# Kernel tuning notes

Hardware: AMD Instinct MI355X
Metric: run time of the kernel (lower is better)

## Reference

```python
import jax, jax.numpy as jnp
import numpy as np

N_NODES = 100000
N_EDGES = 50000
NNZ = 1600000
C_IN = 128
C_OUT = 128
BN_EPS = 1e-5


def setup_inputs() -> dict:
    key = jax.random.key(0)
    k_x, k_ni, k_ei, k_w, k_W, k_b = jax.random.split(key, 6)
    x = jax.random.normal(k_x, (N_NODES, C_IN), dtype=jnp.float32)
    node_idx = jax.random.randint(k_ni, (NNZ,), 0, N_NODES, dtype=jnp.int64)
    edge_idx = jax.random.randint(k_ei, (NNZ,), 0, N_EDGES, dtype=jnp.int64)
    hyperedge_index = jnp.stack([node_idx, edge_idx], axis=0)  # [2, nnz]
    hyperedge_weight = jax.random.uniform(k_w, (N_EDGES,), dtype=jnp.float32)
    W = jax.random.normal(k_W, (C_IN, C_OUT), dtype=jnp.float32) * (1.0 / np.sqrt(C_IN))
    b = jax.random.normal(k_b, (C_OUT,), dtype=jnp.float32) * 0.02
    gamma = jnp.ones((C_OUT,), dtype=jnp.float32)
    beta = jnp.zeros((C_OUT,), dtype=jnp.float32)
    return {"x": x, "hyperedge_index": hyperedge_index,
            "hyperedge_weight": hyperedge_weight, "W": W, "b": b,
            "gamma": gamma, "beta": beta}


def reference(x, hyperedge_index, hyperedge_weight, W, b, gamma, beta):
    # HypergraphConv (PyG semantics): out = D^{-1} H B^{-1} H^T (X W) + b
    # D_v = sum_{e: v in e} w_e  (hyperedge weights enter via node degree),
    # B_e = |e| (number of incident nodes).
    N = x.shape[0]
    E = hyperedge_weight.shape[0]
    node_idx = hyperedge_index[0]
    edge_idx = hyperedge_index[1]

    xt = x @ W  # [N, C_out]

    # Node degree D (weighted) and hyperedge degree B.
    D = jax.ops.segment_sum(hyperedge_weight[edge_idx], node_idx, num_segments=N)
    D_inv = jnp.where(D > 0, 1.0 / D, 0.0)  # inf -> 0
    Bdeg = jax.ops.segment_sum(jnp.ones(edge_idx.shape, dtype=xt.dtype),
                               edge_idx, num_segments=E)
    B_inv = jnp.where(Bdeg > 0, 1.0 / Bdeg, 0.0)

    # node -> hyperedge aggregation: e = B^{-1} sum_{v in e} xt_v
    e_feat = jax.ops.segment_sum(xt[node_idx], edge_idx, num_segments=E)
    e_feat = e_feat * B_inv[:, None]  # [E, C_out]

    # hyperedge -> node aggregation: out_v = D^{-1} sum_{e ni v} e_feat_e
    out = jax.ops.segment_sum(e_feat[edge_idx], node_idx, num_segments=N)
    out = out * D_inv[:, None] + b  # [N, C_out]

    # BatchNorm (training-mode batch statistics over nodes)
    mean = jnp.mean(out, axis=0)
    var = jnp.mean(jnp.square(out - mean), axis=0)  # biased, as BatchNorm1d
    out = (out - mean) * jax.lax.rsqrt(var + BN_EPS) * gamma + beta

    # SiLU activation
    out = out * jax.nn.sigmoid(out)
    # NOTE: original code computes `x = out + x` for the skip but returns `out`,
    # so the skip is a no-op; we faithfully return `out` (use_skip=False here).
    return out
```

## Files before the change

### kernel.cpp

```cpp
#include <hip/hip_runtime.h>
#include <cstdint>
#include <cstddef>

#define CC 128
#define LOG_FINE 7
#define FINE 128
#define CAPE 6144
#define CAPV 3072
#define BIN_TILE 8192

__device__ __forceinline__ unsigned f2b(float f) {
    const unsigned u = __float_as_uint(f);
    return (u + 0x7fffu + ((u >> 16) & 1u)) >> 16;
}
__device__ __forceinline__ float b2f_lo(unsigned u) { return __uint_as_float(u << 16); }
__device__ __forceinline__ float b2f_hi(unsigned u) { return __uint_as_float(u & 0xffff0000u); }

__global__ __launch_bounds__(512) void prep(const int* __restrict__ nidx,
                                            const int* __restrict__ eidx,
                                            int* __restrict__ curE,
                                            int* __restrict__ curV,
                                            unsigned* __restrict__ binnedE,
                                            unsigned* __restrict__ binnedV,
                                            int nnz, int nbE, int nbV, int nbin,
                                            const float4* __restrict__ xin,
                                            uint2* __restrict__ xh, int n4) {
    __shared__ int cntE[512], gposE[512];
    __shared__ int cntV[1024], gposV[1024];
    const int tid = threadIdx.x;
    if (blockIdx.x >= (unsigned)nbin) {
        const int bid = blockIdx.x - nbin;
        const int nblk = gridDim.x - nbin;
        for (int i = bid * 512 + tid; i < n4; i += nblk * 512) {
            const float4 v = xin[i];
            xh[i] = make_uint2(f2b(v.x) | (f2b(v.y) << 16), f2b(v.z) | (f2b(v.w) << 16));
        }
        return;
    }
    for (int i = tid; i < nbE; i += 512) cntE[i] = 0;
    for (int i = tid; i < nbV; i += 512) cntV[i] = 0;
    __syncthreads();
    const int base = blockIdx.x * BIN_TILE;
    int pE[16], rE[16], pV[16], rV[16];
#pragma unroll
    for (int j = 0; j < 16; ++j) {
        const int i = base + tid + j * 512;
        if (i < nnz) {
            const int e = eidx[i], v = nidx[i];
            const int bE = e >> LOG_FINE, bV = v >> LOG_FINE;
            rE[j] = (bE << 16) | atomicAdd(&cntE[bE], 1);
            pE[j] = (v << LOG_FINE) | (e & (FINE - 1));
            rV[j] = (bV << 16) | atomicAdd(&cntV[bV], 1);
            pV[j] = (e << LOG_FINE) | (v & (FINE - 1));
        } else { rE[j] = -1; rV[j] = -1; }
    }
    __syncthreads();
    for (int i = tid; i < nbE; i += 512) {
        const int c = cntE[i];
        gposE[i] = (c > 0) ? atomicAdd(&curE[i], c) : 0;
    }
    for (int i = tid; i < nbV; i += 512) {
        const int c = cntV[i];
        gposV[i] = (c > 0) ? atomicAdd(&curV[i], c) : 0;
    }
    __syncthreads();
#pragma unroll
    for (int j = 0; j < 16; ++j) {
        if (rE[j] >= 0) {
            const int b = rE[j] >> 16;
            binnedE[(size_t)b * CAPE + gposE[b] + (rE[j] & 0xffff)] = (unsigned)pE[j];
        }
        if (rV[j] >= 0) {
            const int b = rV[j] >> 16;
            binnedV[(size_t)b * CAPV + gposV[b] + (rV[j] & 0xffff)] = (unsigned)pV[j];
        }
    }
}

__global__ __launch_bounds__(512) void fill_fineE(const int* __restrict__ cur,
                                                  unsigned* __restrict__ binned,
                                                  int2* __restrict__ rows, int nrows) {
    __shared__ unsigned vals[CAPE];
    __shared__ int scnt[FINE], soff[FINE], sscan[FINE];
    const int tid = threadIdx.x;
    const int b = blockIdx.x;
    const int base = b * CAPE;
    const int cnt = cur[b];
    for (int i = tid; i < cnt; i += 512) vals[i] = binned[base + i];
    if (tid < FINE) scnt[tid] = 0;
    __syncthreads();
    for (int i = tid; i < cnt; i += 512) atomicAdd(&scnt[vals[i] & (FINE - 1)], 1);
    __syncthreads();
    if (tid < FINE) sscan[tid] = scnt[tid];
    __syncthreads();
#pragma unroll
    for (int d = 1; d < FINE; d <<= 1) {
        int t = 0;
        if (tid >= d && tid < FINE) t = sscan[tid - d];
        __syncthreads();
        if (tid < FINE) sscan[tid] += t;
        __syncthreads();
    }
    if (tid < FINE) {
        const int excl = sscan[tid] - scnt[tid];
        soff[tid] = excl;
        const int row = (b << LOG_FINE) + tid;
        if (row < nrows) rows[row] = make_int2(base + excl, base + excl + scnt[tid]);
    }
    __syncthreads();
    for (int i = tid; i < cnt; i += 512) {
        const unsigned p = vals[i];
        const int slot = (int)(p & (FINE - 1));
        const int pos = base + atomicAdd(&soff[slot], 1);
        binned[pos] = p >> LOG_FINE;
    }
}

__global__ __launch_bounds__(512) void fillV_gather(const int* __restrict__ curV,
                                                    unsigned* __restrict__ binnedV,
                                                    const float* __restrict__ hw,
                                                    int2* __restrict__ rowsV,
                                                    float* __restrict__ Dinv,
                                                    int N, int nbV,
                                                    const int2* __restrict__ rowsE,
                                                    const unsigned* __restrict__ binnedE,
                                                    const uint4* __restrict__ xh4,
                                                    uint4* __restrict__ eraw4, int E) {
    __shared__ unsigned vals[CAPV];
    __shared__ int scnt[FINE], soff[FINE], sscan[FINE];
    __shared__ float sd[FINE];
    const int tid = threadIdx.x;
    if (blockIdx.x < (unsigned)nbV) {
        const int b = blockIdx.x;
        const int base = b * CAPV;
        const int cnt = curV[b];
        for (int i = tid; i < cnt; i += 512) vals[i] = binnedV[base + i];
        if (tid < FINE) { scnt[tid] = 0; sd[tid] = 0.f; }
        __syncthreads();
        for (int i = tid; i < cnt; i += 512) atomicAdd(&scnt[vals[i] & (FINE - 1)], 1);
        __syncthreads();
        if (tid < FINE) sscan[tid] = scnt[tid];
        __syncthreads();
#pragma unroll
        for (int d = 1; d < FINE; d <<= 1) {
            int t = 0;
            if (tid >= d && tid < FINE) t = sscan[tid - d];
            __syncthreads();
            if (tid < FINE) sscan[tid] += t;
            __syncthreads();
        }
        if (tid < FINE) {
            const int excl = sscan[tid] - scnt[tid];
            soff[tid] = excl;
            const int row = (b << LOG_FINE) + tid;
            if (row < N) rowsV[row] = make_int2(base + excl, base + excl + scnt[tid]);
        }
        __syncthreads();
        for (int i = tid; i < cnt; i += 512) {
            const unsigned p = vals[i];
            const int slot = (int)(p & (FINE - 1));
            const int e = (int)(p >> LOG_FINE);
            const int pos = base + atomicAdd(&soff[slot], 1);
            binnedV[pos] = (unsigned)e;
            atomicAdd(&sd[slot], hw[e]);
        }
        __syncthreads();
        if (tid < FINE) {
            const int row = (b << LOG_FINE) + tid;
            if (row < N) {
                const float d = sd[tid];
                Dinv[row] = (d > 0.f) ? 1.f / d : 0.f;
            }
        }
        return;
    }
    const int sub = tid >> 5;
    const int half = (tid >> 4) & 1;
    const int q = tid & 15;
    const int e = (blockIdx.x - nbV) * 16 + sub;
    if (e >= E) return;
    const int2 st = rowsE[e];
    const int s = st.x, t = st.y;
    float a[8];
#pragma unroll
    for (int k = 0; k < 8; ++k) a[k] = 0.f;
    int j = s;
    for (; j + 7 < t; j += 8) {
        const int v0 = (int)binnedE[j + 0 + half];
        const int v1 = (int)binnedE[j + 2 + half];
        const int v2 = (int)binnedE[j + 4 + half];
        const int v3 = (int)binnedE[j + 6 + half];
        const uint4 u0 = xh4[(size_t)v0 * 16 + q];
        const uint4 u1 = xh4[(size_t)v1 * 16 + q];
        const uint4 u2 = xh4[(size_t)v2 * 16 + q];
        const uint4 u3 = xh4[(size_t)v3 * 16 + q];
        a[0] += b2f_lo(u0.x) + b2f_lo(u1.x) + b2f_lo(u2.x) + b2f_lo(u3.x);
        a[1] += b2f_hi(u0.x) + b2f_hi(u1.x) + b2f_hi(u2.x) + b2f_hi(u3.x);
        a[2] += b2f_lo(u0.y) + b2f_lo(u1.y) + b2f_lo(u2.y) + b2f_lo(u3.y);
        a[3] += b2f_hi(u0.y) + b2f_hi(u1.y) + b2f_hi(u2.y) + b2f_hi(u3.y);
        a[4] += b2f_lo(u0.z) + b2f_lo(u1.z) + b2f_lo(u2.z) + b2f_lo(u3.z);
        a[5] += b2f_hi(u0.z) + b2f_hi(u1.z) + b2f_hi(u2.z) + b2f_hi(u3.z);
        a[6] += b2f_lo(u0.w) + b2f_lo(u1.w) + b2f_lo(u2.w) + b2f_lo(u3.w);
        a[7] += b2f_hi(u0.w) + b2f_hi(u1.w) + b2f_hi(u2.w) + b2f_hi(u3.w);
    }
    for (; j + 1 < t; j += 2) {
        const int v0 = (int)binnedE[j + half];
        const uint4 u = xh4[(size_t)v0 * 16 + q];
        a[0] += b2f_lo(u.x); a[1] += b2f_hi(u.x);
        a[2] += b2f_lo(u.y); a[3] += b2f_hi(u.y);
        a[4] += b2f_lo(u.z); a[5] += b2f_hi(u.z);
        a[6] += b2f_lo(u.w); a[7] += b2f_hi(u.w);
    }
    if (j < t && half == 0) {
        const uint4 u = xh4[(size_t)binnedE[j] * 16 + q];
        a[0] += b2f_lo(u.x); a[1] += b2f_hi(u.x);
        a[2] += b2f_lo(u.y); a[3] += b2f_hi(u.y);
        a[4] += b2f_lo(u.z); a[5] += b2f_hi(u.z);
        a[6] += b2f_lo(u.w); a[7] += b2f_hi(u.w);
    }
#pragma unroll
    for (int k = 0; k < 8; ++k) a[k] += __shfl_xor(a[k], 16);
    if (half == 0) {
        const float binv = (t > s) ? 1.f / (float)(t - s) : 0.f;
#pragma unroll
        for (int k = 0; k < 8; ++k) a[k] *= binv;
        uint4 o;
        o.x = f2b(a[0]) | (f2b(a[1]) << 16);
        o.y = f2b(a[2]) | (f2b(a[3]) << 16);
        o.z = f2b(a[4]) | (f2b(a[5]) << 16);
        o.w = f2b(a[6]) | (f2b(a[7]) << 16);
        eraw4[(size_t)e * 16 + q] = o;
    }
}

__global__ __launch_bounds__(256) void mm_kernel(const unsigned* __restrict__ A,
                                                 const float* __restrict__ W,
                                                 unsigned* __restrict__ Out, int M) {
    __shared__ float Wl[CC * CC];
    __shared__ float Xl[32 * CC];
    const int tid = threadIdx.x;
    for (int i = tid * 4; i < CC * CC; i += 1024) {
        *(float4*)&Wl[i] = *(const float4*)&W[i];
    }
    const int row0 = blockIdx.x * 32;
    for (int i = tid; i < 2048; i += 256) {
        const int r = i >> 6;
        const int u = i & 63;
        const int row = row0 + r;
        const unsigned val = (row < M) ? A[(size_t)row * 64 + u] : 0u;
        Xl[r * CC + 2 * u]     = b2f_lo(val);
        Xl[r * CC + 2 * u + 1] = b2f_hi(val);
    }
    __syncthreads();
    const int c4 = (tid & 31) * 4;
    const int rg = tid >> 5;
    float4 acc[4];
#pragma unroll
    for (int r = 0; r < 4; ++r) acc[r] = make_float4(0.f, 0.f, 0.f, 0.f);
    for (int k4 = 0; k4 < 32; ++k4) {
        float4 xv[4];
#pragma unroll
        for (int r = 0; r < 4; ++r) xv[r] = *(const float4*)&Xl[(rg + r * 8) * CC + k4 * 4];
#pragma unroll
        for (int kk = 0; kk < 4; ++kk) {
            const float4 w = *(const float4*)&Wl[(k4 * 4 + kk) * CC + c4];
#pragma unroll
            for (int r = 0; r < 4; ++r) {
                const float xs = (&xv[r].x)[kk];
                acc[r].x += xs * w.x; acc[r].y += xs * w.y;
                acc[r].z += xs * w.z; acc[r].w += xs * w.w;
            }
        }
    }
#pragma unroll
    for (int r = 0; r < 4; ++r) {
        const int row = row0 + rg + r * 8;
        if (row < M) {
            *(uint2*)&Out[(size_t)row * 64 + (c4 >> 1)] =
                make_uint2(f2b(acc[r].x) | (f2b(acc[r].y) << 16),
                           f2b(acc[r].z) | (f2b(acc[r].w) << 16));
        }
    }
}

__global__ __launch_bounds__(256) void gather_e2n(const int2* __restrict__ rows,
                                                  const unsigned* __restrict__ lst,
                                                  const uint4* __restrict__ ef4,
                                                  const float* __restrict__ Dinv,
                                                  const float* __restrict__ b,
                                                  float* __restrict__ out, int N) {
    const int sub = threadIdx.x >> 5;
    const int half = (threadIdx.x >> 4) & 1;
    const int q = threadIdx.x & 15;
    const int v = blockIdx.x * 8 + sub;
    if (v >= N) return;
    const int2 st = rows[v];
    const int s = st.x, t = st.y;
    float a[8];
#pragma unroll
    for (int k = 0; k < 8; ++k) a[k] = 0.f;
    int j = s;
    for (; j + 7 < t; j += 8) {
        const int e0 = (int)lst[j + 0 + half];
        const int e1 = (int)lst[j + 2 + half];
        const int e2 = (int)lst[j + 4 + half];
        const int e3 = (int)lst[j + 6 + half];
        const uint4 u0 = ef4[(size_t)e0 * 16 + q];
        const uint4 u1 = ef4[(size_t)e1 * 16 + q];
        const uint4 u2 = ef4[(size_t)e2 * 16 + q];
        const uint4 u3 = ef4[(size_t)e3 * 16 + q];
        a[0] += b2f_lo(u0.x) + b2f_lo(u1.x) + b2f_lo(u2.x) + b2f_lo(u3.x);
        a[1] += b2f_hi(u0.x) + b2f_hi(u1.x) + b2f_hi(u2.x) + b2f_hi(u3.x);
        a[2] += b2f_lo(u0.y) + b2f_lo(u1.y) + b2f_lo(u2.y) + b2f_lo(u3.y);
        a[3] += b2f_hi(u0.y) + b2f_hi(u1.y) + b2f_hi(u2.y) + b2f_hi(u3.y);
        a[4] += b2f_lo(u0.z) + b2f_lo(u1.z) + b2f_lo(u2.z) + b2f_lo(u3.z);
        a[5] += b2f_hi(u0.z) + b2f_hi(u1.z) + b2f_hi(u2.z) + b2f_hi(u3.z);
        a[6] += b2f_lo(u0.w) + b2f_lo(u1.w) + b2f_lo(u2.w) + b2f_lo(u3.w);
        a[7] += b2f_hi(u0.w) + b2f_hi(u1.w) + b2f_hi(u2.w) + b2f_hi(u3.w);
    }
    for (; j + 1 < t; j += 2) {
        const int e0 = (int)lst[j + half];
        const uint4 u = ef4[(size_t)e0 * 16 + q];
        a[0] += b2f_lo(u.x); a[1] += b2f_hi(u.x);
        a[2] += b2f_lo(u.y); a[3] += b2f_hi(u.y);
        a[4] += b2f_lo(u.z); a[5] += b2f_hi(u.z);
        a[6] += b2f_lo(u.w); a[7] += b2f_hi(u.w);
    }
    if (j < t && half == 0) {
        const uint4 u = ef4[(size_t)lst[j] * 16 + q];
        a[0] += b2f_lo(u.x); a[1] += b2f_hi(u.x);
        a[2] += b2f_lo(u.y); a[3] += b2f_hi(u.y);
        a[4] += b2f_lo(u.z); a[5] += b2f_hi(u.z);
        a[6] += b2f_lo(u.w); a[7] += b2f_hi(u.w);
    }
#pragma unroll
    for (int k = 0; k < 8; ++k) a[k] += __shfl_xor(a[k], 16);
    if (half == 0) {
        const float dinv = Dinv[v];
        const float4 b0 = *(const float4*)&b[8 * q];
        const float4 b1 = *(const float4*)&b[8 * q + 4];
        float4 o0, o1;
        o0.x = a[0] * dinv + b0.x; o0.y = a[1] * dinv + b0.y;
        o0.z = a[2] * dinv + b0.z; o0.w = a[3] * dinv + b0.w;
        o1.x = a[4] * dinv + b1.x; o1.y = a[5] * dinv + b1.y;
        o1.z = a[6] * dinv + b1.z; o1.w = a[7] * dinv + b1.w;
        *(float4*)&out[(size_t)v * CC + 8 * q] = o0;
        *(float4*)&out[(size_t)v * CC + 8 * q + 4] = o1;
    }
}

__global__ __launch_bounds__(512) void bn_stats(const float* __restrict__ out,
                                                float* __restrict__ sums, int N) {
    __shared__ float reds[512];
    __shared__ float redq[512];
    const int c = threadIdx.x & 127;
    const int rg = threadIdx.x >> 7;
    float s = 0.f, sq = 0.f;
    for (int v = blockIdx.x * 4 + rg; v < N; v += gridDim.x * 4) {
        const float y = out[(size_t)v * CC + c];
        s += y; sq += y * y;
    }
    reds[threadIdx.x] = s;
    redq[threadIdx.x] = sq;
    __syncthreads();
    if (rg == 0) {
        const float ts = reds[c] + reds[128 + c] + reds[256 + c] + reds[384 + c];
        const float tq = redq[c] + redq[128 + c] + redq[256 + c] + redq[384 + c];
        atomicAdd(&sums[c], ts);
        atomicAdd(&sums[CC + c], tq);
    }
}

__global__ __launch_bounds__(256) void bn_silu(float* __restrict__ out,
                                               const float* __restrict__ sums,
                                               const float* __restrict__ gamma,
                                               const float* __restrict__ beta, int N) {
    const int sub = threadIdx.x >> 5;
    const int lane = threadIdx.x & 31;
    const int c4 = lane * 4;
    const float invN = 1.0f / (float)N;
    const float4 m4 = *(const float4*)&sums[c4];
    const float4 q4 = *(const float4*)&sums[128 + c4];
    const float4 g4 = *(const float4*)&gamma[c4];
    const float4 be4 = *(const float4*)&beta[c4];
    float g[4], bb[4];
#pragma unroll
    for (int k = 0; k < 4; ++k) {
        const float mean = (&m4.x)[k] * invN;
        float var = (&q4.x)[k] * invN - mean * mean;
        var = fmaxf(var, 0.f);
        const float istd = rsqrtf(var + 1e-5f);
        g[k] = (&g4.x)[k] * istd;
        bb[k] = (&be4.x)[k] - mean * g[k];
    }
    for (int v = blockIdx.x * 8 + sub; v < N; v += gridDim.x * 8) {
        float4 y = *(const float4*)&out[(size_t)v * CC + c4];
        float z[4];
#pragma unroll
        for (int k = 0; k < 4; ++k) {
            z[k] = (&y.x)[k] * g[k] + bb[k];
            (&y.x)[k] = z[k] / (1.f + __expf(-z[k]));
        }
        *(float4*)&out[(size_t)v * CC + c4] = y;
    }
}

extern "C" void kernel_launch(void* const* d_in, const int* in_sizes, int n_in,
                              void* d_out, int out_size, void* d_ws, size_t ws_size,
                              hipStream_t stream) {
    const float* x     = (const float*)d_in[0];
    const int*   hidx  = (const int*)d_in[1];
    const float* hw    = (const float*)d_in[2];
    const float* W     = (const float*)d_in[3];
    const float* b     = (const float*)d_in[4];
    const float* gamma = (const float*)d_in[5];
    const float* beta  = (const float*)d_in[6];

    const int N   = in_sizes[0] / CC;
    const int nnz = in_sizes[1] / 2;
    const int E   = in_sizes[2];

    const int* nidx = hidx;
    const int* eidx = hidx + nnz;

    float* out = (float*)d_out;

    const int nbE = (E + FINE - 1) / FINE;
    const int nbV = (N + FINE - 1) / FINE;

    unsigned* ws      = (unsigned*)d_ws;
    unsigned* xh      = ws;
    unsigned* eraw    = xh + (size_t)N * 64;
    unsigned* efeat   = eraw + (size_t)E * 64;
    int2*     rowsE   = (int2*)(efeat + (size_t)E * 64);
    int2*     rowsV   = rowsE + E;
    float*    Dinv    = (float*)(rowsV + N);
    float*    sums    = Dinv + N;
    int*      curE    = (int*)(sums + 256);
    int*      curV    = curE + nbE;
    unsigned* binnedE = (unsigned*)(curV + nbV);
    unsigned* binnedV = binnedE + (size_t)nbE * CAPE;

    hipMemsetAsync(sums, 0, (256 + (size_t)nbE + nbV) * sizeof(int), stream);

    const int nbin = (nnz + BIN_TILE - 1) / BIN_TILE;
    const int ncvt = 256;
    prep<<<nbin + ncvt, 512, 0, stream>>>(nidx, eidx, curE, curV, binnedE, binnedV,
                                          nnz, nbE, nbV, nbin,
                                          (const float4*)x, (uint2*)xh, N * CC / 4);

    fill_fineE<<<nbE, 512, 0, stream>>>(curE, binnedE, rowsE, E);

    fillV_gather<<<nbV + (E + 15) / 16, 512, 0, stream>>>(
        curV, binnedV, hw, rowsV, Dinv, N, nbV,
        rowsE, binnedE, (const uint4*)xh, (uint4*)eraw, E);

    mm_kernel<<<(E + 31) / 32, 256, 0, stream>>>(eraw, W, efeat, E);
    gather_e2n<<<(N + 7) / 8, 256, 0, stream>>>(rowsV, binnedV, (const uint4*)efeat,
                                                Dinv, b, out, N);

    bn_stats<<<512, 512, 0, stream>>>(out, sums, N);
    bn_silu<<<1024, 256, 0, stream>>>(out, sums, gamma, beta, N);
}
```

Baseline: 266.5 us.

## Use bf16 MFMA for edge matmul and fuse BN statistics into gather

Replaces the FP32 LDS-tiled matmul with a bf16 MFMA kernel that reads W from a pre-packed fragment buffer built once by a small prep kernel. The node gather now writes a bf16 intermediate and accumulates per-channel sum and sum-of-squares in shared memory, then adds them into 64 spread global copies. This removes the separate bn_stats pass and the FP32 read/write of the output before BN. The cost is extra bf16 rounding of the pre-BN activations, statistics computed from unrounded values while normalising rounded ones, and many shared-memory atomics per block.

```diff
diff --git a/kernel.cpp b/kernel.cpp
--- a/kernel.cpp
+++ b/kernel.cpp
@@ -8,6 +8,9 @@
 #define CAPE 6144
 #define CAPV 3072
 #define BIN_TILE 8192
+
+typedef __attribute__((ext_vector_type(8))) short bf16x8;
+typedef __attribute__((ext_vector_type(4))) float f32x4;
 
 __device__ __forceinline__ unsigned f2b(float f) {
     const unsigned u = __float_as_uint(f);
@@ -75,6 +78,24 @@
             binnedV[(size_t)b * CAPV + gposV[b] + (rV[j] & 0xffff)] = (unsigned)pV[j];
         }
     }
+}
+
+__global__ __launch_bounds__(256) void bfrag_prep(const float* __restrict__ W,
+                                                  uint4* __restrict__ Bfrag) {
+    const int idx = blockIdx.x * 256 + threadIdx.x;
+    if (idx >= 2048) return;
+    const int lane = idx & 63, t = idx >> 6;
+    const int kk = t >> 3, nt = t & 7;
+    const int k0 = kk * 32 + (lane >> 4) * 8;
+    const int n = nt * 16 + (lane & 15);
+    unsigned r[4];
+#pragma unroll
+    for (int p = 0; p < 4; ++p) {
+        const float w0 = W[(size_t)(k0 + 2 * p) * CC + n];
+        const float w1 = W[(size_t)(k0 + 2 * p + 1) * CC + n];
+        r[p] = f2b(w0) | (f2b(w1) << 16);
+    }
+    Bfrag[idx] = make_uint4(r[0], r[1], r[2], r[3]);
 }
 
 __global__ __launch_bounds__(512) void fill_fineE(const int* __restrict__ cur,
@@ -233,175 +254,164 @@
     }
 }
 
-__global__ __launch_bounds__(256) void mm_kernel(const unsigned* __restrict__ A,
-                                                 const float* __restrict__ W,
-                                                 unsigned* __restrict__ Out, int M) {
-    __shared__ float Wl[CC * CC];
-    __shared__ float Xl[32 * CC];
+__global__ __launch_bounds__(256) void mm_mfma(const uint4* __restrict__ A4,
+                                               const uint4* __restrict__ Bfrag,
+                                               unsigned short* __restrict__ Out, int M) {
+    const int lane = threadIdx.x & 63;
+    const int wave = threadIdx.x >> 6;
+    const int row0 = blockIdx.x * 64 + wave * 16;
+    const int g = lane >> 4;
+    const int c = lane & 15;
+    const int arow = row0 + c;
+    uint4 a[4];
+#pragma unroll
+    for (int kk = 0; kk < 4; ++kk) {
+        a[kk] = (arow < M) ? A4[(size_t)arow * 16 + kk * 4 + g]
+                           : make_uint4(0u, 0u, 0u, 0u);
+    }
+    f32x4 acc[8];
+#pragma unroll
+    for (int nt = 0; nt < 8; ++nt) acc[nt] = (f32x4){0.f, 0.f, 0.f, 0.f};
+#pragma unroll
+    for (int nt = 0; nt < 8; ++nt) {
+#pragma unroll
+        for (int kk = 0; kk < 4; ++kk) {
+            const uint4 bv = Bfrag[(kk * 8 + nt) * 64 + lane];
+            acc[nt] = __builtin_amdgcn_mfma_f32_16x16x32_bf16(
+                *(const bf16x8*)&a[kk], *(const bf16x8*)&bv, acc[nt], 0, 0, 0);
+        }
+    }
+#pragma unroll
+    for (int nt = 0; nt < 8; ++nt) {
+#pragma unroll
+        for (int r = 0; r < 4; ++r) {
+            const int row = row0 + g * 4 + r;
+            if (row < M) Out[(size_t)row * CC + nt * 16 + c] = (unsigned short)f2b(acc[nt][r]);
+        }
+    }
+}
+
+__global__ __launch_bounds__(256) void gather_e2n_bn(const int2* __restrict__ rows,
+                                                     const unsigned* __restrict__ lst,
+                                                     const uint4* __restrict__ ef4,
+                                                     const float* __restrict__ Dinv,
+                                                     const float* __restrict__ b,
+                                                     uint4* __restrict__ oh,
+                                                     float* __restrict__ copies, int N) {
+    __shared__ float bl[256];
     const int tid = threadIdx.x;
-    for (int i = tid * 4; i < CC * CC; i += 1024) {
-        *(float4*)&Wl[i] = *(const float4*)&W[i];
-    }
-    const int row0 = blockIdx.x * 32;
-    for (int i = tid; i < 2048; i += 256) {
-        const int r = i >> 6;
-        const int u = i & 63;
-        const int row = row0 + r;
-        const unsigned val = (row < M) ? A[(size_t)row * 64 + u] : 0u;
-        Xl[r * CC + 2 * u]     = b2f_lo(val);
-        Xl[r * CC + 2 * u + 1] = b2f_hi(val);
-    }
-    __syncthreads();
-    const int c4 = (tid & 31) * 4;
-    const int rg = tid >> 5;
-    float4 acc[4];
-#pragma unroll
-    for (int r = 0; r < 4; ++r) acc[r] = make_float4(0.f, 0.f, 0.f, 0.f);
-    for (int k4 = 0; k4 < 32; ++k4) {
-        float4 xv[4];
-#pragma unroll
-        for (int r = 0; r < 4; ++r) xv[r] = *(const float4*)&Xl[(rg + r * 8) * CC + k4 * 4];
-#pragma unroll
-        for (int kk = 0; kk < 4; ++kk) {
-            const float4 w = *(const float4*)&Wl[(k4 * 4 + kk) * CC + c4];
-#pragma unroll
-            for (int r = 0; r < 4; ++r) {
-                const float xs = (&xv[r].x)[kk];
-                acc[r].x += xs * w.x; acc[r].y += xs * w.y;
-                acc[r].z += xs * w.z; acc[r].w += xs * w.w;
+    bl[tid] = 0.f;
+    __syncthreads();
+    const int sub = tid >> 5;
+    const int half = (tid >> 4) & 1;
+    const int q = tid & 15;
+    const int v = blockIdx.x * 8 + sub;
+    if (v < N) {
+        const int2 st = rows[v];
+        const int s = st.x, t = st.y;
+        float a[8];
+#pragma unroll
+        for (int k = 0; k < 8; ++k) a[k] = 0.f;
+        int j = s;
+        for (; j + 7 < t; j += 8) {
+            const int e0 = (int)lst[j + 0 + half];
+            const int e1 = (int)lst[j + 2 + half];
+            const int e2 = (int)lst[j + 4 + half];
+            const int e3 = (int)lst[j + 6 + half];
+            const uint4 u0 = ef4[(size_t)e0 * 16 + q];
+            const uint4 u1 = ef4[(size_t)e1 * 16 + q];
+            const uint4 u2 = ef4[(size_t)e2 * 16 + q];
+            const uint4 u3 = ef4[(size_t)e3 * 16 + q];
+            a[0] += b2f_lo(u0.x) + b2f_lo(u1.x) + b2f_lo(u2.x) + b2f_lo(u3.x);
+            a[1] += b2f_hi(u0.x) + b2f_hi(u1.x) + b2f_hi(u2.x) + b2f_hi(u3.x);
+            a[2] += b2f_lo(u0.y) + b2f_lo(u1.y) + b2f_lo(u2.y) + b2f_lo(u3.y);
+            a[3] += b2f_hi(u0.y) + b2f_hi(u1.y) + b2f_hi(u2.y) + b2f_hi(u3.y);
+            a[4] += b2f_lo(u0.z) + b2f_lo(u1.z) + b2f_lo(u2.z) + b2f_lo(u3.z);
+            a[5] += b2f_hi(u0.z) + b2f_hi(u1.z) + b2f_hi(u2.z) + b2f_hi(u3.z);
+            a[6] += b2f_lo(u0.w) + b2f_lo(u1.w) + b2f_lo(u2.w) + b2f_lo(u3.w);
+            a[7] += b2f_hi(u0.w) + b2f_hi(u1.w) + b2f_hi(u2.w) + b2f_hi(u3.w);
+        }
+        for (; j + 1 < t; j += 2) {
+            const int e0 = (int)lst[j + half];
+            const uint4 u = ef4[(size_t)e0 * 16 + q];
+            a[0] += b2f_lo(u.x); a[1] += b2f_hi(u.x);
+            a[2] += b2f_lo(u.y); a[3] += b2f_hi(u.y);
+            a[4] += b2f_lo(u.z); a[5] += b2f_hi(u.z);
+            a[6] += b2f_lo(u.w); a[7] += b2f_hi(u.w);
+        }
+        if (j < t && half == 0) {
+            const uint4 u = ef4[(size_t)lst[j] * 16 + q];
+            a[0] += b2f_lo(u.x); a[1] += b2f_hi(u.x);
+            a[2] += b2f_lo(u.y); a[3] += b2f_hi(u.y);
+            a[4] += b2f_lo(u.z); a[5] += b2f_hi(u.z);
+            a[6] += b2f_lo(u.w); a[7] += b2f_hi(u.w);
+        }
+#pragma unroll
+        for (int k = 0; k < 8; ++k) a[k] += __shfl_xor(a[k], 16);
+        if (half == 0) {
+            const float dinv = Dinv[v];
+            const float4 b0 = *(const float4*)&b[8 * q];
+            const float4 b1 = *(const float4*)&b[8 * q + 4];
+            float o[8];
+            o[0] = a[0] * dinv + b0.x; o[1] = a[1] * dinv + b0.y;
+            o[2] = a[2] * dinv + b0.z; o[3] = a[3] * dinv + b0.w;
+            o[4] = a[4] * dinv + b1.x; o[5] = a[5] * dinv + b1.y;
+            o[6] = a[6] * dinv + b1.z; o[7] = a[7] * dinv + b1.w;
+            uint4 ov;
+            ov.x = f2b(o[0]) | (f2b(o[1]) << 16);
+            ov.y = f2b(o[2]) | (f2b(o[3]) << 16);
+            ov.z = f2b(o[4]) | (f2b(o[5]) << 16);
+            ov.w = f2b(o[6]) | (f2b(o[7]) << 16);
+            oh[(size_t)v * 16 + q] = ov;
+#pragma unroll
+            for (int k = 0; k < 8; ++k) {
+                atomicAdd(&bl[8 * q + k], o[k]);
+                atomicAdd(&bl[128 + 8 * q + k], o[k] * o[k]);
             }
         }
     }
-#pragma unroll
-    for (int r = 0; r < 4; ++r) {
-        const int row = row0 + rg + r * 8;
-        if (row < M) {
-            *(uint2*)&Out[(size_t)row * 64 + (c4 >> 1)] =
-                make_uint2(f2b(acc[r].x) | (f2b(acc[r].y) << 16),
-                           f2b(acc[r].z) | (f2b(acc[r].w) << 16));
-        }
-    }
-}
-
-__global__ __launch_bounds__(256) void gather_e2n(const int2* __restrict__ rows,
-                                                  const unsigned* __restrict__ lst,
-                                                  const uint4* __restrict__ ef4,
-                                                  const float* __restrict__ Dinv,
-                                                  const float* __restrict__ b,
-                                                  float* __restrict__ out, int N) {
-    const int sub = threadIdx.x >> 5;
-    const int half = (threadIdx.x >> 4) & 1;
-    const int q = threadIdx.x & 15;
-    const int v = blockIdx.x * 8 + sub;
-    if (v >= N) return;
-    const int2 st = rows[v];
-    const int s = st.x, t = st.y;
-    float a[8];
-#pragma unroll
-    for (int k = 0; k < 8; ++k) a[k] = 0.f;
-    int j = s;
-    for (; j + 7 < t; j += 8) {
-        const int e0 = (int)lst[j + 0 + half];
-        const int e1 = (int)lst[j + 2 + half];
-        const int e2 = (int)lst[j + 4 + half];
-        const int e3 = (int)lst[j + 6 + half];
-        const uint4 u0 = ef4[(size_t)e0 * 16 + q];
-        const uint4 u1 = ef4[(size_t)e1 * 16 + q];
-        const uint4 u2 = ef4[(size_t)e2 * 16 + q];
-        const uint4 u3 = ef4[(size_t)e3 * 16 + q];
-        a[0] += b2f_lo(u0.x) + b2f_lo(u1.x) + b2f_lo(u2.x) + b2f_lo(u3.x);
-        a[1] += b2f_hi(u0.x) + b2f_hi(u1.x) + b2f_hi(u2.x) + b2f_hi(u3.x);
-        a[2] += b2f_lo(u0.y) + b2f_lo(u1.y) + b2f_lo(u2.y) + b2f_lo(u3.y);
-        a[3] += b2f_hi(u0.y) + b2f_hi(u1.y) + b2f_hi(u2.y) + b2f_hi(u3.y);
-        a[4] += b2f_lo(u0.z) + b2f_lo(u1.z) + b2f_lo(u2.z) + b2f_lo(u3.z);
-        a[5] += b2f_hi(u0.z) + b2f_hi(u1.z) + b2f_hi(u2.z) + b2f_hi(u3.z);
-        a[6] += b2f_lo(u0.w) + b2f_lo(u1.w) + b2f_lo(u2.w) + b2f_lo(u3.w);
-        a[7] += b2f_hi(u0.w) + b2f_hi(u1.w) + b2f_hi(u2.w) + b2f_hi(u3.w);
-    }
-    for (; j + 1 < t; j += 2) {
-        const int e0 = (int)lst[j + half];
-        const uint4 u = ef4[(size_t)e0 * 16 + q];
-        a[0] += b2f_lo(u.x); a[1] += b2f_hi(u.x);
-        a[2] += b2f_lo(u.y); a[3] += b2f_hi(u.y);
-        a[4] += b2f_lo(u.z); a[5] += b2f_hi(u.z);
-        a[6] += b2f_lo(u.w); a[7] += b2f_hi(u.w);
-    }
-    if (j < t && half == 0) {
-        const uint4 u = ef4[(size_t)lst[j] * 16 + q];
-        a[0] += b2f_lo(u.x); a[1] += b2f_hi(u.x);
-        a[2] += b2f_lo(u.y); a[3] += b2f_hi(u.y);
-        a[4] += b2f_lo(u.z); a[5] += b2f_hi(u.z);
-        a[6] += b2f_lo(u.w); a[7] += b2f_hi(u.w);
-    }
-#pragma unroll
-    for (int k = 0; k < 8; ++k) a[k] += __shfl_xor(a[k], 16);
-    if (half == 0) {
-        const float dinv = Dinv[v];
-        const float4 b0 = *(const float4*)&b[8 * q];
-        const float4 b1 = *(const float4*)&b[8 * q + 4];
-        float4 o0, o1;
-        o0.x = a[0] * dinv + b0.x; o0.y = a[1] * dinv + b0.y;
-        o0.z = a[2] * dinv + b0.z; o0.w = a[3] * dinv + b0.w;
-        o1.x = a[4] * dinv + b1.x; o1.y = a[5] * dinv + b1.y;
-        o1.z = a[6] * dinv + b1.z; o1.w = a[7] * dinv + b1.w;
-        *(float4*)&out[(size_t)v * CC + 8 * q] = o0;
-        *(float4*)&out[(size_t)v * CC + 8 * q + 4] = o1;
-    }
-}
-
-__global__ __launch_bounds__(512) void bn_stats(const float* __restrict__ out,
-                                                float* __restrict__ sums, int N) {
-    __shared__ float reds[512];
-    __shared__ float redq[512];
-    const int c = threadIdx.x & 127;
-    const int rg = threadIdx.x >> 7;
-    float s = 0.f, sq = 0.f;
-    for (int v = blockIdx.x * 4 + rg; v < N; v += gridDim.x * 4) {
-        const float y = out[(size_t)v * CC + c];
-        s += y; sq += y * y;
-    }
-    reds[threadIdx.x] = s;
-    redq[threadIdx.x] = sq;
-    __syncthreads();
-    if (rg == 0) {
-        const float ts = reds[c] + reds[128 + c] + reds[256 + c] + reds[384 + c];
-        const float tq = redq[c] + redq[128 + c] + redq[256 + c] + redq[384 + c];
-        atomicAdd(&sums[c], ts);
-        atomicAdd(&sums[CC + c], tq);
-    }
-}
-
-__global__ __launch_bounds__(256) void bn_silu(float* __restrict__ out,
-                                               const float* __restrict__ sums,
+    __syncthreads();
+    atomicAdd(&copies[(blockIdx.x & 63) * 256 + tid], bl[tid]);
+}
+
+__global__ __launch_bounds__(256) void bn_silu(const uint2* __restrict__ oh2,
+                                               const float* __restrict__ copies,
                                                const float* __restrict__ gamma,
-                                               const float* __restrict__ beta, int N) {
-    const int sub = threadIdx.x >> 5;
-    const int lane = threadIdx.x & 31;
+                                               const float* __restrict__ beta,
+                                               float* __restrict__ out, int N) {
+    __shared__ float sl[256];
+    const int tid = threadIdx.x;
+    float s = 0.f;
+#pragma unroll 8
+    for (int i = 0; i < 64; ++i) s += copies[i * 256 + tid];
+    sl[tid] = s;
+    __syncthreads();
+    const int sub = tid >> 5;
+    const int lane = tid & 31;
     const int c4 = lane * 4;
     const float invN = 1.0f / (float)N;
-    const float4 m4 = *(const float4*)&sums[c4];
-    const float4 q4 = *(const float4*)&sums[128 + c4];
-    const float4 g4 = *(const float4*)&gamma[c4];
-    const float4 be4 = *(const float4*)&beta[c4];
     float g[4], bb[4];
 #pragma unroll
     for (int k = 0; k < 4; ++k) {
-        const float mean = (&m4.x)[k] * invN;
-        float var = (&q4.x)[k] * invN - mean * mean;
+        const float mean = sl[c4 + k] * invN;
+        float var = sl[128 + c4 + k] * invN - mean * mean;
         var = fmaxf(var, 0.f);
         const float istd = rsqrtf(var + 1e-5f);
-        g[k] = (&g4.x)[k] * istd;
-        bb[k] = (&be4.x)[k] - mean * g[k];
+        g[k] = gamma[c4 + k] * istd;
+        bb[k] = beta[c4 + k] - mean * g[k];
     }
     for (int v = blockIdx.x * 8 + sub; v < N; v += gridDim.x * 8) {
-        float4 y = *(const float4*)&out[(size_t)v * CC + c4];
-        float z[4];
+        const uint2 u = oh2[(size_t)v * 32 + lane];
+        float y[4];
+        y[0] = b2f_lo(u.x); y[1] = b2f_hi(u.x);
+        y[2] = b2f_lo(u.y); y[3] = b2f_hi(u.y);
+        float4 o;
 #pragma unroll
         for (int k = 0; k < 4; ++k) {
-            z[k] = (&y.x)[k] * g[k] + bb[k];
-            (&y.x)[k] = z[k] / (1.f + __expf(-z[k]));
-        }
-        *(float4*)&out[(size_t)v * CC + c4] = y;
+            const float z = y[k] * g[k] + bb[k];
+            (&o.x)[k] = z / (1.f + __expf(-z));
+        }
+        *(float4*)&out[(size_t)v * CC + c4] = o;
     }
 }
 
@@ -435,19 +445,22 @@
     int2*     rowsE   = (int2*)(efeat + (size_t)E * 64);
     int2*     rowsV   = rowsE + E;
     float*    Dinv    = (float*)(rowsV + N);
-    float*    sums    = Dinv + N;
-    int*      curE    = (int*)(sums + 256);
+    float*    copies  = Dinv + N;
+    int*      curE    = (int*)(copies + 64 * 256);
     int*      curV    = curE + nbE;
     unsigned* binnedE = (unsigned*)(curV + nbV);
     unsigned* binnedV = binnedE + (size_t)nbE * CAPE;
-
-    hipMemsetAsync(sums, 0, (256 + (size_t)nbE + nbV) * sizeof(int), stream);
+    uintptr_t bfaddr  = (uintptr_t)(binnedV + (size_t)nbV * CAPV);
+    uint4*    Bfrag   = (uint4*)((bfaddr + 15) & ~(uintptr_t)15);
+
+    hipMemsetAsync(copies, 0, (64 * 256 + (size_t)nbE + nbV) * sizeof(int), stream);
 
     const int nbin = (nnz + BIN_TILE - 1) / BIN_TILE;
     const int ncvt = 256;
     prep<<<nbin + ncvt, 512, 0, stream>>>(nidx, eidx, curE, curV, binnedE, binnedV,
                                           nnz, nbE, nbV, nbin,
                                           (const float4*)x, (uint2*)xh, N * CC / 4);
+    bfrag_prep<<<8, 256, 0, stream>>>(W, Bfrag);
 
     fill_fineE<<<nbE, 512, 0, stream>>>(curE, binnedE, rowsE, E);
 
@@ -455,10 +468,11 @@
         curV, binnedV, hw, rowsV, Dinv, N, nbV,
         rowsE, binnedE, (const uint4*)xh, (uint4*)eraw, E);
 
-    mm_kernel<<<(E + 31) / 32, 256, 0, stream>>>(eraw, W, efeat, E);
-    gather_e2n<<<(N + 7) / 8, 256, 0, stream>>>(rowsV, binnedV, (const uint4*)efeat,
-                                                Dinv, b, out, N);
-
-    bn_stats<<<512, 512, 0, stream>>>(out, sums, N);
-    bn_silu<<<1024, 256, 0, stream>>>(out, sums, gamma, beta, N);
-}
+    mm_mfma<<<(E + 63) / 64, 256, 0, stream>>>((const uint4*)eraw, Bfrag,
+                                               (unsigned short*)efeat, E);
+
+    gather_e2n_bn<<<(N + 7) / 8, 256, 0, stream>>>(rowsV, binnedV, (const uint4*)efeat,
+                                                   Dinv, b, (uint4*)xh, copies, N);
+
+    bn_silu<<<1024, 256, 0, stream>>>((const uint2*)xh, copies, gamma, beta, out, N);
+}
```

After: 310.4 us. 1.16x slower.
